# Kernel tuning notes

Measured on AMD Instinct MI355X. Metric: run time of the kernel, lower is better.

## Reference

```python
import jax, jax.numpy as jnp
import numpy as np

EPS = 1e-06

def elu_feature_map(x):
    return jax.nn.elu(x) + 1.0

def setup_inputs() -> dict:
    key = jax.random.key(0)
    kq, kk, kv = jax.random.split(key, 3)
    shape = (4, 8, 4096, 64)  # [B, H, L, D]
    return {
        "queries": jax.random.normal(kq, shape, dtype=jnp.float32),
        "keys": jax.random.normal(kk, shape, dtype=jnp.float32),
        "values": jax.random.normal(kv, shape, dtype=jnp.float32),
    }

def reference(queries, keys, values):
    Q = elu_feature_map(queries)            # [b,h,l,d]
    K = elu_feature_map(keys)               # [b,h,l,d]
    v_length = values.shape[-2]
    values_n = values / v_length            # [b,h,l,v]
    KV = jnp.einsum('bhld,bhlv->bhdv', K, values_n)          # [b,h,d,v]
    Z = 1.0 / (jnp.einsum('bhld,bhd->bhl', Q, K.sum(axis=-2)) + EPS)  # [b,h,l]
    out = jnp.einsum('bhld,bhdv,bhl->bhlv', Q, KV, Z) * v_length
    return out
```

## Files before the change

kernel.cpp:

```cpp
#include <hip/hip_runtime.h>


#define LSEQ   4096
#define DDIM   64
#define NHEAD  32
#define CHUNKS 32
#define ROWSB  (LSEQ / CHUNKS)
#define TILE   16
#define WSPH   (DDIM * DDIM + DDIM)
#define WSPH4  (WSPH / 4)

__device__ __forceinline__ float fmap(float x) {
    return x > 0.0f ? (x + 1.0f) : __expf(x);
}

__device__ __forceinline__ void fma4(float4& a, float s, const float4& b) {
    a.x = fmaf(s, b.x, a.x);
    a.y = fmaf(s, b.y, a.y);
    a.z = fmaf(s, b.z, a.z);
    a.w = fmaf(s, b.w, a.w);
}

__global__ __launch_bounds__(256) void la_kv_kernel(
    const float* __restrict__ Kg, const float* __restrict__ Vg,
    float* __restrict__ ws)
{
    __shared__ float klds[TILE * DDIM];
    __shared__ float vlds[TILE * DDIM];
    __shared__ float red[WSPH];

    const int t    = threadIdx.x;
    const int wave = t >> 6;
    const int lane = t & 63;
    const int dq   = lane >> 3;
    const int vq   = lane & 7;

    const int bh    = blockIdx.x / CHUNKS;
    const int chunk = blockIdx.x % CHUNKS;
    const size_t base = (size_t)bh * LSEQ * DDIM + (size_t)chunk * ROWSB * DDIM;
    const float* Kb = Kg + base;
    const float* Vb = Vg + base;
    const float invL = 1.0f / (float)LSEQ;

    float acc[8][8];
    float ksum[8];
#pragma unroll
    for (int i = 0; i < 8; ++i) {
        ksum[i] = 0.0f;
#pragma unroll
        for (int j = 0; j < 8; ++j) acc[i][j] = 0.0f;
    }

    for (int tile = 0; tile < ROWSB / TILE; ++tile) {
        __syncthreads();
        float4 kx = ((const float4*)(Kb + tile * TILE * DDIM))[t];
        kx.x = fmap(kx.x); kx.y = fmap(kx.y); kx.z = fmap(kx.z); kx.w = fmap(kx.w);
        ((float4*)klds)[t] = kx;
        float4 vx = ((const float4*)(Vb + tile * TILE * DDIM))[t];
        vx.x *= invL; vx.y *= invL; vx.z *= invL; vx.w *= invL;
        ((float4*)vlds)[t] = vx;
        __syncthreads();

#pragma unroll
        for (int r = 0; r < 4; ++r) {
            const int l = wave * 4 + r;
            const float4 ka = *(const float4*)(klds + l * DDIM + dq * 8);
            const float4 kb = *(const float4*)(klds + l * DDIM + dq * 8 + 4);
            const float4 va = *(const float4*)(vlds + l * DDIM + vq * 4);
            const float4 vb = *(const float4*)(vlds + l * DDIM + 32 + vq * 4);
            const float kk[8] = {ka.x, ka.y, ka.z, ka.w, kb.x, kb.y, kb.z, kb.w};
            const float vv[8] = {va.x, va.y, va.z, va.w, vb.x, vb.y, vb.z, vb.w};
#pragma unroll
            for (int i = 0; i < 8; ++i) {
                ksum[i] += kk[i];
#pragma unroll
                for (int j = 0; j < 8; ++j)
                    acc[i][j] = fmaf(kk[i], vv[j], acc[i][j]);
            }
        }
    }

    for (int w = 0; w < 4; ++w) {
        __syncthreads();
        if (wave == w) {
#pragma unroll
            for (int i = 0; i < 8; ++i) {
                const int d = dq * 8 + i;
                float* p = red + d * DDIM + vq * 4;
                float4 lo = make_float4(acc[i][0], acc[i][1], acc[i][2], acc[i][3]);
                float4 hi = make_float4(acc[i][4], acc[i][5], acc[i][6], acc[i][7]);
                if (w != 0) {
                    const float4 plo = *(const float4*)p;
                    const float4 phi = *(const float4*)(p + 32);
                    lo.x += plo.x; lo.y += plo.y; lo.z += plo.z; lo.w += plo.w;
                    hi.x += phi.x; hi.y += phi.y; hi.z += phi.z; hi.w += phi.w;
                }
                *(float4*)p = lo;
                *(float4*)(p + 32) = hi;
            }
            if (vq == 0) {
                float* p = red + DDIM * DDIM + dq * 8;
                float4 s0 = make_float4(ksum[0], ksum[1], ksum[2], ksum[3]);
                float4 s1 = make_float4(ksum[4], ksum[5], ksum[6], ksum[7]);
                if (w != 0) {
                    const float4 p0 = *(const float4*)p;
                    const float4 p1 = *(const float4*)(p + 4);
                    s0.x += p0.x; s0.y += p0.y; s0.z += p0.z; s0.w += p0.w;
                    s1.x += p1.x; s1.y += p1.y; s1.z += p1.z; s1.w += p1.w;
                }
                *(float4*)p = s0;
                *(float4*)(p + 4) = s1;
            }
        }
    }
    __syncthreads();

    float4* dst = (float4*)(ws + (size_t)blockIdx.x * WSPH);
    const float4* src = (const float4*)red;
    for (int i = t; i < WSPH4; i += 256)
        dst[i] = src[i];
}

__global__ __launch_bounds__(256) void la_reduce_kernel(
    const float* __restrict__ ws, float* __restrict__ kvout)
{
    const int h   = blockIdx.x / 5;
    const int seg = blockIdx.x % 5;
    const int t   = threadIdx.x;
    if (t >= 208) return;
    const int i4 = seg * 208 + t;

    const float4* base = (const float4*)(ws + (size_t)h * CHUNKS * WSPH) + i4;
    float4 acc = make_float4(0.f, 0.f, 0.f, 0.f);
#pragma unroll 8
    for (int p = 0; p < CHUNKS; ++p) {
        const float4 x = base[(size_t)p * WSPH4];
        acc.x += x.x; acc.y += x.y; acc.z += x.z; acc.w += x.w;
    }
    ((float4*)(kvout + (size_t)h * WSPH))[i4] = acc;
}

#define QSTRIDE 68

__global__ __launch_bounds__(256) void la_out_kernel(
    const float* __restrict__ Qg, const float* __restrict__ kvin,
    float* __restrict__ out)
{
    __shared__ float kvlds[DDIM * DDIM];
    __shared__ float ksl[DDIM];
    __shared__ float qlds[128 * QSTRIDE];
    __shared__ float zs[128];

    const int t    = threadIdx.x;
    const int bh   = blockIdx.x >> 5;
    const int tile = blockIdx.x & 31;
    const size_t base = (size_t)bh * LSEQ * DDIM + (size_t)tile * 128 * DDIM;
    const float* Qb = Qg + base;
    float* Ob = out + base;

    const float4* wsrc = (const float4*)(kvin + (size_t)bh * WSPH);
    for (int i = t; i < 1040; i += 256) {
        const float4 x = wsrc[i];
        if (i < 1024) ((float4*)kvlds)[i] = x;
        else          ((float4*)ksl)[i - 1024] = x;
    }

#pragma unroll
    for (int i = 0; i < 8; ++i) {
        const int o = t + i * 256;
        float4 q = ((const float4*)Qb)[o];
        q.x = fmap(q.x); q.y = fmap(q.y); q.z = fmap(q.z); q.w = fmap(q.w);
        const int row = o >> 4;
        const int c4  = o & 15;
        *(float4*)(qlds + row * QSTRIDE + c4 * 4) = q;
    }
    __syncthreads();

    {
        const int row  = t >> 1;
        const int half = t & 1;
        float s = 0.0f;
#pragma unroll
        for (int i = 0; i < 8; ++i) {
            const float4 q  = *(const float4*)(qlds + row * QSTRIDE + half * 32 + i * 4);
            const float4 ks = *(const float4*)(ksl + half * 32 + i * 4);
            s += q.x * ks.x + q.y * ks.y + q.z * ks.z + q.w * ks.w;
        }
        s += __shfl_xor(s, 1);
        if (half == 0) zs[row] = (float)LSEQ / (s + 1e-6f);
    }
    __syncthreads();

    const int vq = t & 7;
    const int rg = t >> 3;
    float4 accL[4], accH[4];
#pragma unroll
    for (int r = 0; r < 4; ++r) {
        accL[r] = make_float4(0.f, 0.f, 0.f, 0.f);
        accH[r] = make_float4(0.f, 0.f, 0.f, 0.f);
    }

    for (int d4 = 0; d4 < 16; ++d4) {
        float4 kvlo[4], kvhi[4];
#pragma unroll
        for (int i = 0; i < 4; ++i) {
            kvlo[i] = *(const float4*)(kvlds + (d4 * 4 + i) * DDIM + vq * 4);
            kvhi[i] = *(const float4*)(kvlds + (d4 * 4 + i) * DDIM + 32 + vq * 4);
        }
#pragma unroll
        for (int r = 0; r < 4; ++r) {
            const float4 q = *(const float4*)(qlds + (rg * 4 + r) * QSTRIDE + d4 * 4);
            fma4(accL[r], q.x, kvlo[0]);
            fma4(accL[r], q.y, kvlo[1]);
            fma4(accL[r], q.z, kvlo[2]);
            fma4(accL[r], q.w, kvlo[3]);
            fma4(accH[r], q.x, kvhi[0]);
            fma4(accH[r], q.y, kvhi[1]);
            fma4(accH[r], q.z, kvhi[2]);
            fma4(accH[r], q.w, kvhi[3]);
        }
    }

#pragma unroll
    for (int r = 0; r < 4; ++r) {
        const int row = rg * 4 + r;
        const float z = zs[row];
        float4 o = accL[r];
        o.x *= z; o.y *= z; o.z *= z; o.w *= z;
        *(float4*)(Ob + row * DDIM + vq * 4) = o;
        o = accH[r];
        o.x *= z; o.y *= z; o.z *= z; o.w *= z;
        *(float4*)(Ob + row * DDIM + 32 + vq * 4) = o;
    }
}

extern "C" void kernel_launch(void* const* d_in, const int* in_sizes, int n_in,
                              void* d_out, int out_size, void* d_ws, size_t ws_size,
                              hipStream_t stream) {
    const float* q = (const float*)d_in[0];
    const float* k = (const float*)d_in[1];
    const float* v = (const float*)d_in[2];
    float* o  = (float*)d_out;
    float* ws = (float*)d_ws;
    float* kvfinal = ws + (size_t)NHEAD * CHUNKS * WSPH;

    hipLaunchKernelGGL(la_kv_kernel, dim3(NHEAD * CHUNKS), dim3(256), 0, stream,
                       k, v, ws);
    hipLaunchKernelGGL(la_reduce_kernel, dim3(NHEAD * 5), dim3(256), 0, stream,
                       ws, kvfinal);
    hipLaunchKernelGGL(la_out_kernel, dim3(NHEAD * (LSEQ / 128)), dim3(256), 0, stream,
                       q, kvfinal, o);
}
```

Baseline: 57.14 us.

## Drop LDS staging, use packed FP32 FMA, fuse normalizer into output loop

The KV kernel now has each wave read K/V rows directly from global memory into registers and accumulate with packed two-wide FMA, removing LDS staging and per-tile barriers. The output kernel reads Q directly per thread, computes the denominator inside the main loop, and handles 8 rows per thread over 256-row tiles, removing the Q LDS buffer and an extra barrier. Since the 1/L and *L factors cancel, both scalings are dropped. Redundant global loads across lanes and higher register pressure are the tradeoffs.

```diff
diff --git a/kernel.cpp b/kernel.cpp
--- a/kernel.cpp
+++ b/kernel.cpp
@@ -4,29 +4,24 @@
 #define LSEQ   4096
 #define DDIM   64
 #define NHEAD  32
-#define CHUNKS 32
-#define ROWSB  (LSEQ / CHUNKS)
-#define TILE   16
+#define K1CH   32
+#define K1ROWS (LSEQ / K1CH)
 #define WSPH   (DDIM * DDIM + DDIM)
 #define WSPH4  (WSPH / 4)
 
+typedef float f2 __attribute__((ext_vector_type(2)));
+
 __device__ __forceinline__ float fmap(float x) {
     return x > 0.0f ? (x + 1.0f) : __expf(x);
 }
-
-__device__ __forceinline__ void fma4(float4& a, float s, const float4& b) {
-    a.x = fmaf(s, b.x, a.x);
-    a.y = fmaf(s, b.y, a.y);
-    a.z = fmaf(s, b.z, a.z);
-    a.w = fmaf(s, b.w, a.w);
+__device__ __forceinline__ f2 pkfma(f2 a, f2 b, f2 c) {
+    return __builtin_elementwise_fma(a, b, c);
 }
 
 __global__ __launch_bounds__(256) void la_kv_kernel(
     const float* __restrict__ Kg, const float* __restrict__ Vg,
     float* __restrict__ ws)
 {
-    __shared__ float klds[TILE * DDIM];
-    __shared__ float vlds[TILE * DDIM];
     __shared__ float red[WSPH];
 
     const int t    = threadIdx.x;
@@ -35,47 +30,42 @@
     const int dq   = lane >> 3;
     const int vq   = lane & 7;
 
-    const int bh    = blockIdx.x / CHUNKS;
-    const int chunk = blockIdx.x % CHUNKS;
-    const size_t base = (size_t)bh * LSEQ * DDIM + (size_t)chunk * ROWSB * DDIM;
-    const float* Kb = Kg + base;
-    const float* Vb = Vg + base;
-    const float invL = 1.0f / (float)LSEQ;
-
-    float acc[8][8];
+    const int bh    = blockIdx.x / K1CH;
+    const int chunk = blockIdx.x % K1CH;
+    const size_t base = (size_t)bh * LSEQ * DDIM + (size_t)chunk * K1ROWS * DDIM
+                      + (size_t)wave * 32 * DDIM;
+    const float* Kp = Kg + base;
+    const float* Vp = Vg + base;
+
+    f2 acc[8][4];
     float ksum[8];
 #pragma unroll
     for (int i = 0; i < 8; ++i) {
         ksum[i] = 0.0f;
 #pragma unroll
-        for (int j = 0; j < 8; ++j) acc[i][j] = 0.0f;
-    }
-
-    for (int tile = 0; tile < ROWSB / TILE; ++tile) {
-        __syncthreads();
-        float4 kx = ((const float4*)(Kb + tile * TILE * DDIM))[t];
-        kx.x = fmap(kx.x); kx.y = fmap(kx.y); kx.z = fmap(kx.z); kx.w = fmap(kx.w);
-        ((float4*)klds)[t] = kx;
-        float4 vx = ((const float4*)(Vb + tile * TILE * DDIM))[t];
-        vx.x *= invL; vx.y *= invL; vx.z *= invL; vx.w *= invL;
-        ((float4*)vlds)[t] = vx;
-        __syncthreads();
-
-#pragma unroll
-        for (int r = 0; r < 4; ++r) {
-            const int l = wave * 4 + r;
-            const float4 ka = *(const float4*)(klds + l * DDIM + dq * 8);
-            const float4 kb = *(const float4*)(klds + l * DDIM + dq * 8 + 4);
-            const float4 va = *(const float4*)(vlds + l * DDIM + vq * 4);
-            const float4 vb = *(const float4*)(vlds + l * DDIM + 32 + vq * 4);
-            const float kk[8] = {ka.x, ka.y, ka.z, ka.w, kb.x, kb.y, kb.z, kb.w};
-            const float vv[8] = {va.x, va.y, va.z, va.w, vb.x, vb.y, vb.z, vb.w};
+        for (int j = 0; j < 4; ++j) acc[i][j] = (f2)(0.0f);
+    }
+
+#pragma unroll 1
+    for (int g = 0; g < 4; ++g) {
+        const float* kR = Kp + g * 8 * DDIM;
+        const float* vR = Vp + g * 8 * DDIM;
+#pragma unroll
+        for (int r = 0; r < 8; ++r) {
+            const float4 ka = *(const float4*)(kR + r * DDIM + dq * 8);
+            const float4 kb = *(const float4*)(kR + r * DDIM + dq * 8 + 4);
+            const float4 va = *(const float4*)(vR + r * DDIM + vq * 4);
+            const float4 vb = *(const float4*)(vR + r * DDIM + 32 + vq * 4);
+            const float kk[8] = {fmap(ka.x), fmap(ka.y), fmap(ka.z), fmap(ka.w),
+                                 fmap(kb.x), fmap(kb.y), fmap(kb.z), fmap(kb.w)};
+            const f2 vv[4] = {{va.x, va.y}, {va.z, va.w}, {vb.x, vb.y}, {vb.z, vb.w}};
 #pragma unroll
             for (int i = 0; i < 8; ++i) {
                 ksum[i] += kk[i];
-#pragma unroll
-                for (int j = 0; j < 8; ++j)
-                    acc[i][j] = fmaf(kk[i], vv[j], acc[i][j]);
+                const f2 ki = {kk[i], kk[i]};
+#pragma unroll
+                for (int j = 0; j < 4; ++j)
+                    acc[i][j] = pkfma(ki, vv[j], acc[i][j]);
             }
         }
     }
@@ -87,8 +77,8 @@
             for (int i = 0; i < 8; ++i) {
                 const int d = dq * 8 + i;
                 float* p = red + d * DDIM + vq * 4;
-                float4 lo = make_float4(acc[i][0], acc[i][1], acc[i][2], acc[i][3]);
-                float4 hi = make_float4(acc[i][4], acc[i][5], acc[i][6], acc[i][7]);
+                float4 lo = make_float4(acc[i][0].x, acc[i][0].y, acc[i][1].x, acc[i][1].y);
+                float4 hi = make_float4(acc[i][2].x, acc[i][2].y, acc[i][3].x, acc[i][3].y);
                 if (w != 0) {
                     const float4 plo = *(const float4*)p;
                     const float4 phi = *(const float4*)(p + 32);
@@ -130,17 +120,15 @@
     if (t >= 208) return;
     const int i4 = seg * 208 + t;
 
-    const float4* base = (const float4*)(ws + (size_t)h * CHUNKS * WSPH) + i4;
+    const float4* base = (const float4*)(ws + (size_t)h * K1CH * WSPH) + i4;
     float4 acc = make_float4(0.f, 0.f, 0.f, 0.f);
 #pragma unroll 8
-    for (int p = 0; p < CHUNKS; ++p) {
+    for (int p = 0; p < K1CH; ++p) {
         const float4 x = base[(size_t)p * WSPH4];
         acc.x += x.x; acc.y += x.y; acc.z += x.z; acc.w += x.w;
     }
     ((float4*)(kvout + (size_t)h * WSPH))[i4] = acc;
 }
-
-#define QSTRIDE 68
 
 __global__ __launch_bounds__(256) void la_out_kernel(
     const float* __restrict__ Qg, const float* __restrict__ kvin,
@@ -148,89 +136,71 @@
 {
     __shared__ float kvlds[DDIM * DDIM];
     __shared__ float ksl[DDIM];
-    __shared__ float qlds[128 * QSTRIDE];
-    __shared__ float zs[128];
 
     const int t    = threadIdx.x;
-    const int bh   = blockIdx.x >> 5;
-    const int tile = blockIdx.x & 31;
-    const size_t base = (size_t)bh * LSEQ * DDIM + (size_t)tile * 128 * DDIM;
-    const float* Qb = Qg + base;
-    float* Ob = out + base;
+    const int bh   = blockIdx.x >> 4;
+    const int tile = blockIdx.x & 15;
+    const size_t base = (size_t)bh * LSEQ * DDIM + (size_t)tile * 256 * DDIM;
 
     const float4* wsrc = (const float4*)(kvin + (size_t)bh * WSPH);
-    for (int i = t; i < 1040; i += 256) {
+    for (int i = t; i < WSPH4; i += 256) {
         const float4 x = wsrc[i];
         if (i < 1024) ((float4*)kvlds)[i] = x;
         else          ((float4*)ksl)[i - 1024] = x;
     }
-
-#pragma unroll
-    for (int i = 0; i < 8; ++i) {
-        const int o = t + i * 256;
-        float4 q = ((const float4*)Qb)[o];
-        q.x = fmap(q.x); q.y = fmap(q.y); q.z = fmap(q.z); q.w = fmap(q.w);
-        const int row = o >> 4;
-        const int c4  = o & 15;
-        *(float4*)(qlds + row * QSTRIDE + c4 * 4) = q;
-    }
     __syncthreads();
 
-    {
-        const int row  = t >> 1;
-        const int half = t & 1;
-        float s = 0.0f;
-#pragma unroll
-        for (int i = 0; i < 8; ++i) {
-            const float4 q  = *(const float4*)(qlds + row * QSTRIDE + half * 32 + i * 4);
-            const float4 ks = *(const float4*)(ksl + half * 32 + i * 4);
-            s += q.x * ks.x + q.y * ks.y + q.z * ks.z + q.w * ks.w;
-        }
-        s += __shfl_xor(s, 1);
-        if (half == 0) zs[row] = (float)LSEQ / (s + 1e-6f);
-    }
-    __syncthreads();
-
+    const int rg = t >> 3;
     const int vq = t & 7;
-    const int rg = t >> 3;
-    float4 accL[4], accH[4];
-#pragma unroll
-    for (int r = 0; r < 4; ++r) {
-        accL[r] = make_float4(0.f, 0.f, 0.f, 0.f);
-        accH[r] = make_float4(0.f, 0.f, 0.f, 0.f);
-    }
-
+    const float* qrow = Qg + base + (size_t)rg * 8 * DDIM;
+    float*       orow = out + base + (size_t)rg * 8 * DDIM;
+
+    f2 acc[8][4];
+    float den[8];
+#pragma unroll
+    for (int r = 0; r < 8; ++r) {
+        den[r] = 0.0f;
+#pragma unroll
+        for (int j = 0; j < 4; ++j) acc[r][j] = (f2)(0.0f);
+    }
+
+#pragma unroll 1
     for (int d4 = 0; d4 < 16; ++d4) {
-        float4 kvlo[4], kvhi[4];
+        f2 kL[4][2], kH[4][2];
 #pragma unroll
         for (int i = 0; i < 4; ++i) {
-            kvlo[i] = *(const float4*)(kvlds + (d4 * 4 + i) * DDIM + vq * 4);
-            kvhi[i] = *(const float4*)(kvlds + (d4 * 4 + i) * DDIM + 32 + vq * 4);
-        }
-#pragma unroll
-        for (int r = 0; r < 4; ++r) {
-            const float4 q = *(const float4*)(qlds + (rg * 4 + r) * QSTRIDE + d4 * 4);
-            fma4(accL[r], q.x, kvlo[0]);
-            fma4(accL[r], q.y, kvlo[1]);
-            fma4(accL[r], q.z, kvlo[2]);
-            fma4(accL[r], q.w, kvlo[3]);
-            fma4(accH[r], q.x, kvhi[0]);
-            fma4(accH[r], q.y, kvhi[1]);
-            fma4(accH[r], q.z, kvhi[2]);
-            fma4(accH[r], q.w, kvhi[3]);
-        }
-    }
-
-#pragma unroll
-    for (int r = 0; r < 4; ++r) {
-        const int row = rg * 4 + r;
-        const float z = zs[row];
-        float4 o = accL[r];
-        o.x *= z; o.y *= z; o.z *= z; o.w *= z;
-        *(float4*)(Ob + row * DDIM + vq * 4) = o;
-        o = accH[r];
-        o.x *= z; o.y *= z; o.z *= z; o.w *= z;
-        *(float4*)(Ob + row * DDIM + 32 + vq * 4) = o;
+            const float4 a = *(const float4*)(kvlds + (d4 * 4 + i) * DDIM + vq * 4);
+            const float4 b = *(const float4*)(kvlds + (d4 * 4 + i) * DDIM + 32 + vq * 4);
+            kL[i][0] = (f2){a.x, a.y}; kL[i][1] = (f2){a.z, a.w};
+            kH[i][0] = (f2){b.x, b.y}; kH[i][1] = (f2){b.z, b.w};
+        }
+        const float4 ks4 = *(const float4*)(ksl + d4 * 4);
+#pragma unroll
+        for (int r = 0; r < 8; ++r) {
+            float4 q = *(const float4*)(qrow + r * DDIM + d4 * 4);
+            q.x = fmap(q.x); q.y = fmap(q.y); q.z = fmap(q.z); q.w = fmap(q.w);
+            den[r] += q.x * ks4.x + q.y * ks4.y + q.z * ks4.z + q.w * ks4.w;
+            const float qa[4] = {q.x, q.y, q.z, q.w};
+#pragma unroll
+            for (int i = 0; i < 4; ++i) {
+                const f2 qb = {qa[i], qa[i]};
+                acc[r][0] = pkfma(qb, kL[i][0], acc[r][0]);
+                acc[r][1] = pkfma(qb, kL[i][1], acc[r][1]);
+                acc[r][2] = pkfma(qb, kH[i][0], acc[r][2]);
+                acc[r][3] = pkfma(qb, kH[i][1], acc[r][3]);
+            }
+        }
+    }
+
+#pragma unroll
+    for (int r = 0; r < 8; ++r) {
+        const float z = 1.0f / (den[r] + 1e-6f);
+        float4 lo = make_float4(acc[r][0].x * z, acc[r][0].y * z,
+                                acc[r][1].x * z, acc[r][1].y * z);
+        float4 hi = make_float4(acc[r][2].x * z, acc[r][2].y * z,
+                                acc[r][3].x * z, acc[r][3].y * z);
+        *(float4*)(orow + r * DDIM + vq * 4) = lo;
+        *(float4*)(orow + r * DDIM + 32 + vq * 4) = hi;
     }
 }
 
@@ -242,12 +212,12 @@
     const float* v = (const float*)d_in[2];
     float* o  = (float*)d_out;
     float* ws = (float*)d_ws;
-    float* kvfinal = ws + (size_t)NHEAD * CHUNKS * WSPH;
-
-    hipLaunchKernelGGL(la_kv_kernel, dim3(NHEAD * CHUNKS), dim3(256), 0, stream,
+    float* kvfinal = ws + (size_t)NHEAD * K1CH * WSPH;
+
+    hipLaunchKernelGGL(la_kv_kernel, dim3(NHEAD * K1CH), dim3(256), 0, stream,
                        k, v, ws);
     hipLaunchKernelGGL(la_reduce_kernel, dim3(NHEAD * 5), dim3(256), 0, stream,
                        ws, kvfinal);
-    hipLaunchKernelGGL(la_out_kernel, dim3(NHEAD * (LSEQ / 128)), dim3(256), 0, stream,
+    hipLaunchKernelGGL(la_out_kernel, dim3(NHEAD * 16), dim3(256), 0, stream,
                        q, kvfinal, o);
 }
```

Measured after the change: 79.37 us. 1.39x slower.
